# Kernel optimization log

Measured on AMD Instinct MI355X. Metric: run time of the kernel, lower is better.

Reference implementation:

```python
import jax, jax.numpy as jnp
import numpy as np
from jax import lax

N, CIN, COUT = 10000, 64, 32
RADIUS = 0.07
K = 32            # cap on neighbors per query (radius search truncated to K nearest)
KSIZE = 3         # kernel_size = [3,3,3]
NCELLS = KSIZE ** 3

# 8 trilinear corner offsets
_OFFS = np.array([[i, j, k] for i in (0, 1) for j in (0, 1) for k in (0, 1)], dtype=np.int32)  # (8,3)
_STRIDE = np.array([KSIZE * KSIZE, KSIZE, 1], dtype=np.int32)


def setup_inputs() -> dict:
    key = jax.random.key(0)
    k1, k2, k3 = jax.random.split(key, 3)
    points = jax.random.uniform(k1, (N, 3), dtype=jnp.float32)
    feats = jax.random.normal(k2, (N, CIN), dtype=jnp.float32)
    # ContinuousConv kernel: [3,3,3,Cin,Cout] flattened to [27,Cin,Cout]
    W = jax.random.normal(k3, (NCELLS, CIN, COUT), dtype=jnp.float32) * 0.05
    b = jnp.zeros((COUT,), dtype=jnp.float32)
    return {"feats": feats, "points": points, "W": W, "b": b}


def _neighbors(points):
    # squared pairwise distances (N,N); radius search truncated to K nearest
    sq = jnp.sum(points * points, axis=-1)
    d2 = sq[:, None] + sq[None, :] - 2.0 * (points @ points.T)
    neg_d2, idx = lax.top_k(-d2, K)           # (N,K)
    valid = (-neg_d2) <= RADIUS * RADIUS      # (N,K) bool
    return idx, valid


def _cconv(feats, points, W, b, idx, valid):
    nb_pos = points[idx]                      # (N,K,3) gather
    rel = (nb_pos - points[:, None, :]) / RADIUS   # normalized by half-extent -> unit ball
    # ball_to_cube_radial: v -> v * ||v||_2 / ||v||_inf  (0 at origin)
    l2 = jnp.linalg.norm(rel, axis=-1, keepdims=True)
    linf = jnp.max(jnp.abs(rel), axis=-1, keepdims=True)
    t = jnp.where(linf > 0, rel * (l2 / jnp.maximum(linf, 1e-12)), 0.0)  # in [-1,1]^3
    # map to kernel grid coords in [0, KSIZE-1]
    coords = (t + 1.0) * 0.5 * (KSIZE - 1)    # (N,K,3)
    c0 = jnp.clip(jnp.floor(coords), 0, KSIZE - 2)
    f = coords - c0                            # trilinear fractions, (N,K,3)
    offs = jnp.asarray(_OFFS)                  # (8,3)
    # trilinear weights (N,K,8)
    fw = jnp.where(offs[None, None] == 1, f[:, :, None, :], 1.0 - f[:, :, None, :])
    w8 = jnp.prod(fw, axis=-1)
    # flattened corner cell indices (N,K,8)
    cidx = jnp.sum((c0[:, :, None, :].astype(jnp.int32) + offs) * jnp.asarray(_STRIDE), axis=-1)
    onehot = jax.nn.one_hot(cidx, NCELLS, dtype=feats.dtype)        # (N,K,8,27)
    wmass = jnp.einsum('nke,nkej->nkj', w8, onehot)                 # (N,K,27)
    wmass = wmass * valid[:, :, None].astype(feats.dtype)
    nb_feats = feats[idx]                                           # (N,K,Cin)
    A = jnp.einsum('nkj,nkf->njf', wmass, nb_feats)                 # (N,27,Cin)
    out = jnp.einsum('njf,jfo->no', A, W)                           # (N,Cout)
    # normalize=True: divide by neighbor importance sum (count, window=None)
    nn = jnp.sum(valid.astype(feats.dtype), axis=-1)
    out = out / jnp.maximum(nn, 1.0)[:, None] + b
    return out


@jax.jit
def reference(feats, points, W, b):
    idx, valid = _neighbors(points)
    return _cconv(feats, points, W, b, idx, valid)
```

## Files before the change

kernel.cpp:

```cpp
#include <hip/hip_runtime.h>
#include <math.h>

#define N_PTS   10000
#define CIN     64
#define COUT    32
#define KCAP    32
#define RADIUSF 0.07f
#define NCELLS  27
#define QB      4
#define MAXC    48
#define GRES    14
#define GCELLS  (GRES * GRES * GRES)
#define CPAD    72
#define NSCAT   40
#define WT_ELEMS (NCELLS * COUT * CIN)

typedef __attribute__((ext_vector_type(8))) short         bf16x8_t;
typedef __attribute__((ext_vector_type(4))) float         f32x4_t;

__device__ __forceinline__ void cell_coords(float x, float y, float z,
                                            int& cx, int& cy, int& cz) {
    cx = (int)(x * (float)GRES); if (cx > GRES - 1) cx = GRES - 1; if (cx < 0) cx = 0;
    cy = (int)(y * (float)GRES); if (cy > GRES - 1) cy = GRES - 1; if (cy < 0) cy = 0;
    cz = (int)(z * (float)GRES); if (cz > GRES - 1) cz = GRES - 1; if (cz < 0) cz = 0;
}

__device__ __forceinline__ unsigned int f2bf_u(float x) {
    unsigned int u = __float_as_uint(x);
    return (u + 0x7FFFu + ((u >> 16) & 1u)) >> 16;
}

__global__ __launch_bounds__(1024) void k1_hist_scan(
    const float* __restrict__ pts,
    int* __restrict__ offsets,
    int* __restrict__ cursor)
{
    __shared__ int s_hist[GCELLS];
    __shared__ int s_wsum[16];
    const int t = threadIdx.x;
    const int lane = t & 63;
    const int wv   = t >> 6;

    for (int i = t; i < GCELLS; i += 1024) s_hist[i] = 0;
    __syncthreads();
    for (int i = t; i < N_PTS; i += 1024) {
        int cx, cy, cz;
        cell_coords(pts[3 * i], pts[3 * i + 1], pts[3 * i + 2], cx, cy, cz);
        atomicAdd(&s_hist[(cx * GRES + cy) * GRES + cz], 1);
    }
    __syncthreads();

    const int c0 = t * 3;
    int v0 = (c0 + 0 < GCELLS) ? s_hist[c0 + 0] : 0;
    int v1 = (c0 + 1 < GCELLS) ? s_hist[c0 + 1] : 0;
    int v2 = (c0 + 2 < GCELLS) ? s_hist[c0 + 2] : 0;
    const int local = v0 + v1 + v2;
    int inc = local;
    #pragma unroll
    for (int d = 1; d < 64; d <<= 1) {
        int up = __shfl_up(inc, d);
        if (lane >= d) inc += up;
    }
    if (lane == 63) s_wsum[wv] = inc;
    __syncthreads();
    if (t == 0) {
        int run = 0;
        #pragma unroll
        for (int i = 0; i < 16; ++i) { int tmp = s_wsum[i]; s_wsum[i] = run; run += tmp; }
    }
    __syncthreads();
    int base = s_wsum[wv] + (inc - local);
    if (c0 + 0 < GCELLS) { offsets[c0 + 0] = base; cursor[c0 + 0] = base; base += v0; }
    if (c0 + 1 < GCELLS) { offsets[c0 + 1] = base; cursor[c0 + 1] = base; base += v1; }
    if (c0 + 2 < GCELLS) { offsets[c0 + 2] = base; cursor[c0 + 2] = base; base += v2; }
    if (t == 0) offsets[GCELLS] = N_PTS;
}

__global__ __launch_bounds__(256) void k2_scatter_wt(
    const float* __restrict__ pts,
    const float* __restrict__ W,
    int*   __restrict__ cursor,
    int*   __restrict__ sorted,
    float* __restrict__ pts_s,
    unsigned short* __restrict__ Wt)
{
    const int b = blockIdx.x;
    const int t = threadIdx.x;

    if (b < NSCAT) {
        const int per = N_PTS / NSCAT;
        const int lo = b * per;
        const int hi = lo + per;
        for (int i = lo + t; i < hi; i += 256) {
            float x = pts[3 * i + 0], y = pts[3 * i + 1], z = pts[3 * i + 2];
            int cx, cy, cz;
            cell_coords(x, y, z, cx, cy, cz);
            int cell = (cx * GRES + cy) * GRES + cz;
            int pos = atomicAdd(&cursor[cell], 1);
            sorted[pos] = i;
            pts_s[3 * pos + 0] = x;
            pts_s[3 * pos + 1] = y;
            pts_s[3 * pos + 2] = z;
        }
    } else {
        __shared__ float tile[CIN * 33];
        const int cell = b - NSCAT;
        for (int idx = t; idx < CIN * COUT; idx += 256) {
            int f = idx >> 5, o = idx & 31;
            tile[f * 33 + o] = W[cell * (CIN * COUT) + idx];
        }
        __syncthreads();
        for (int idx = t; idx < CIN * COUT; idx += 256) {
            int o = idx >> 6, f = idx & 63;
            Wt[cell * (CIN * COUT) + idx] = (unsigned short)f2bf_u(tile[f * 33 + o]);
        }
    }
}

__global__ __launch_bounds__(256) void cconv_grid_mfma_kernel(
    const float* __restrict__ feats,
    const unsigned short* __restrict__ Wt,
    const float* __restrict__ bias,
    const int*   __restrict__ offsets,
    const int*   __restrict__ sorted,
    const float* __restrict__ pts_s,
    float* __restrict__ out)
{
    const int tid  = threadIdx.x;
    const int lane = tid & 63;
    const int wave = tid >> 6;

    __shared__ __align__(16) unsigned short sAb[QB][NCELLS + 1][CPAD];
    __shared__ __align__(16) float s_pool[QB][4][MAXC];
    __shared__ int   s_idx[QB][MAXC];
    __shared__ int   s_org[QB][MAXC];
    __shared__ int   s_sel[QB][KCAP];
    __shared__ int   s_cnt[QB];
    __shared__ int   s_qi[QB];
    __shared__ int   s_nn[QB];

    if (lane == 0) s_cnt[wave] = 0;

    const int q_flat = blockIdx.x * QB + wave;
    const int qi = sorted[q_flat];
    const float qx = pts_s[3 * q_flat + 0];
    const float qy = pts_s[3 * q_flat + 1];
    const float qz = pts_s[3 * q_flat + 2];
    const float sqn = qx * qx + qy * qy + qz * qz;
    const float r2 = RADIUSF * RADIUSF;

    int cx, cy, cz;
    cell_coords(qx, qy, qz, cx, cy, cz);

    int zlo = cz - 1; if (zlo < 0) zlo = 0;
    int zhi = cz + 1; if (zhi > GRES - 1) zhi = GRES - 1;
    int ss[9], sl[9];
    #pragma unroll
    for (int dxi = 0; dxi < 3; ++dxi) {
        #pragma unroll
        for (int dyi = 0; dyi < 3; ++dyi) {
            const int ii = dxi * 3 + dyi;
            int cxx = cx + dxi - 1, cyy = cy + dyi - 1;
            bool ok = (cxx >= 0) && (cxx <= GRES - 1) && (cyy >= 0) && (cyy <= GRES - 1);
            int row = ((ok ? cxx : 0) * GRES + (ok ? cyy : 0)) * GRES;
            int s = offsets[row + zlo];
            int e = offsets[row + zhi + 1];
            ss[ii] = s;
            sl[ii] = ok ? (e - s) : 0;
        }
    }
    int cum[10];
    cum[0] = 0;
    #pragma unroll
    for (int ii = 0; ii < 9; ++ii) cum[ii + 1] = cum[ii] + sl[ii];
    const int T = cum[9];

    for (int t = lane; t < T; t += 64) {
        int gidx = 0;
        #pragma unroll
        for (int ii = 0; ii < 9; ++ii) {
            bool in = (t >= cum[ii]) && (t < cum[ii + 1]);
            int cand = ss[ii] + (t - cum[ii]);
            gidx = in ? cand : gidx;
        }
        float x = pts_s[3 * gidx + 0];
        float y = pts_s[3 * gidx + 1];
        float z = pts_s[3 * gidx + 2];
        float sqj = x * x + y * y + z * z;
        float dot = qx * x + qy * y + qz * z;
        float d2 = (sqn + sqj) - 2.0f * dot;
        if (d2 <= r2) {
            int pos = atomicAdd(&s_cnt[wave], 1);
            if (pos < MAXC) {
                s_pool[wave][0][pos] = d2;
                s_pool[wave][1][pos] = x;
                s_pool[wave][2][pos] = y;
                s_pool[wave][3][pos] = z;
                s_idx[wave][pos] = gidx;
            }
        }
    }

    int M = s_cnt[wave]; if (M > MAXC) M = MAXC;
    const int cnt = (M > KCAP) ? KCAP : M;
    const bool over = (M > KCAP);

    if (lane < M) s_org[wave][lane] = sorted[s_idx[wave][lane]];

    if (over) {
        if (lane < M) {
            float dc = s_pool[wave][0][lane];
            int   ic = s_org[wave][lane];
            int rank = 0;
            for (int m = 0; m < M; ++m) {
                float dm = s_pool[wave][0][m];
                int   im = s_org[wave][m];
                rank += (dm < dc || (dm == dc && im < ic)) ? 1 : 0;
            }
            if (rank < KCAP) s_sel[wave][rank] = lane;
        }
    }
    if (lane == 0) { s_qi[wave] = qi; s_nn[wave] = cnt; }

    float* w9w = (float*)&sAb[wave][0][0];
    if (lane < cnt) {
        int slot = over ? s_sel[wave][lane] : lane;
        float x = s_pool[wave][1][slot];
        float y = s_pool[wave][2][slot];
        float z = s_pool[wave][3][slot];
        int   j = s_org[wave][slot];
        float rx = (x - qx) / RADIUSF;
        float ry = (y - qy) / RADIUSF;
        float rz = (z - qz) / RADIUSF;
        float l2 = sqrtf(rx * rx + ry * ry + rz * rz);
        float ax = fabsf(rx), ay = fabsf(ry), az = fabsf(rz);
        float linf = fmaxf(fmaxf(ax, ay), az);
        float s = (linf > 0.0f) ? (l2 / fmaxf(linf, 1e-12f)) : 0.0f;
        float tx = rx * s, ty = ry * s, tz = rz * s;
        float cxf = (tx + 1.0f) * 0.5f * 2.0f;
        float cyf = (ty + 1.0f) * 0.5f * 2.0f;
        float czf = (tz + 1.0f) * 0.5f * 2.0f;
        float c0x = fminf(fmaxf(floorf(cxf), 0.0f), 1.0f);
        float c0y = fminf(fmaxf(floorf(cyf), 0.0f), 1.0f);
        float c0z = fminf(fmaxf(floorf(czf), 0.0f), 1.0f);
        float fx = cxf - c0x;
        float fy = cyf - c0y;
        float fz = czf - c0z;
        int i0 = (int)c0x, i1 = (int)c0y, i2 = (int)c0z;
        float gx0 = 1.0f - fx, gx1 = fx;
        float gy0 = 1.0f - fy, gy1 = fy;
        float gz0 = 1.0f - fz, gz1 = fz;
        float* wp = w9w + lane * 12;
        wp[0] = i0 ? 0.0f : gx0;  wp[1] = i0 ? gx0 : gx1;  wp[2] = i0 ? gx1 : 0.0f;
        wp[3] = i1 ? 0.0f : gy0;  wp[4] = i1 ? gy0 : gy1;  wp[5] = i1 ? gy1 : 0.0f;
        wp[6] = i2 ? 0.0f : gz0;  wp[7] = i2 ? gz0 : gz1;  wp[8] = i2 ? gz1 : 0.0f;
        wp[9] = __int_as_float(j * CIN);
    }

    float a[NCELLS];
    #pragma unroll
    for (int c = 0; c < NCELLS; ++c) a[c] = 0.0f;

    if (cnt > 0) {
        float fvA = feats[__float_as_int(w9w[9]) + lane];
        float fvB = 0.0f;
        if (cnt > 1) fvB = feats[__float_as_int(w9w[12 + 9]) + lane];
        for (int k = 0; k < cnt; ++k) {
            const float* wp = w9w + k * 12;
            float wxv[3] = {wp[0], wp[1], wp[2]};
            float wyv[3] = {wp[3], wp[4], wp[5]};
            float wz0 = wp[6], wz1 = wp[7], wz2 = wp[8];
            float fv_cur = fvA;
            fvA = fvB;
            if (k + 2 < cnt) fvB = feats[__float_as_int(w9w[(k + 2) * 12 + 9]) + lane];
            float pzv[3] = {wz0 * fv_cur, wz1 * fv_cur, wz2 * fv_cur};
            #pragma unroll
            for (int ci = 0; ci < 3; ++ci) {
                #pragma unroll
                for (int cj = 0; cj < 3; ++cj) {
                    float wxy = wxv[ci] * wyv[cj];
                    #pragma unroll
                    for (int ck = 0; ck < 3; ++ck) {
                        a[ci * 9 + cj * 3 + ck] = fmaf(wxy, pzv[ck], a[ci * 9 + cj * 3 + ck]);
                    }
                }
            }
        }
    }
    #pragma unroll
    for (int c = 0; c < NCELLS; ++c) sAb[wave][c][lane] = (unsigned short)f2bf_u(a[c]);
    sAb[wave][NCELLS][lane] = 0;
    __syncthreads();

    float (*sC)[QB][COUT] = (float (*)[QB][COUT])&s_pool[0][0][0];
    f32x4_t acc0 = {0.f, 0.f, 0.f, 0.f};
    f32x4_t acc1 = {0.f, 0.f, 0.f, 0.f};
    const int r  = lane & 15;
    const int kg = lane >> 4;
    #pragma unroll
    for (int it = 0; it < 14; ++it) {
        const int s5 = wave + it * 4;
        const int c  = s5 >> 1;
        const int f0 = (s5 & 1) << 5;
        const int cw = (c < NCELLS) ? c : 0;
        bf16x8_t af = {};
        if (r < QB) af = *(const bf16x8_t*)&sAb[r][c][f0 + kg * 8];
        const unsigned short* wp0 = Wt + ((cw * COUT + r     ) * CIN + f0 + kg * 8);
        const unsigned short* wp1 = Wt + ((cw * COUT + 16 + r) * CIN + f0 + kg * 8);
        bf16x8_t bf0 = *(const bf16x8_t*)wp0;
        bf16x8_t bf1 = *(const bf16x8_t*)wp1;
        acc0 = __builtin_amdgcn_mfma_f32_16x16x32_bf16(af, bf0, acc0, 0, 0, 0);
        acc1 = __builtin_amdgcn_mfma_f32_16x16x32_bf16(af, bf1, acc1, 0, 0, 0);
    }
    if (lane < 16) {
        #pragma unroll
        for (int j = 0; j < QB; ++j) {
            sC[wave][j][lane]      = acc0[j];
            sC[wave][j][16 + lane] = acc1[j];
        }
    }
    __syncthreads();

    if (tid < QB * COUT) {
        int q = tid >> 5, o = tid & 31;
        float v = sC[0][q][o] + sC[1][q][o] + sC[2][q][o] + sC[3][q][o];
        float nn = (float)s_nn[q];
        out[s_qi[q] * COUT + o] = v / fmaxf(nn, 1.0f) + bias[o];
    }
}

__global__ __launch_bounds__(64) void cconv_fused_kernel(
    const float* __restrict__ feats,
    const float* __restrict__ points,
    const float* __restrict__ W,
    const float* __restrict__ bias,
    float* __restrict__ out)
{
    const int n    = blockIdx.x;
    const int lane = threadIdx.x;

    __shared__ float sA[NCELLS][CIN];
    __shared__ float s_d2[128];
    __shared__ int   s_idx[128];
    __shared__ int   s_rank[128];
    __shared__ int   s_sel[KCAP];
    __shared__ int   s_cnt;

    if (lane == 0) s_cnt = 0;
    for (int c = lane; c < NCELLS * CIN; c += 64) ((float*)sA)[c] = 0.0f;
    __syncthreads();

    const float qx = points[3 * n + 0];
    const float qy = points[3 * n + 1];
    const float qz = points[3 * n + 2];
    const float sqn = qx * qx + qy * qy + qz * qz;
    const float r2 = RADIUSF * RADIUSF;

    for (int j = lane; j < N_PTS; j += 64) {
        float x = points[3 * j + 0];
        float y = points[3 * j + 1];
        float z = points[3 * j + 2];
        float sqj = x * x + y * y + z * z;
        float dot = qx * x + qy * y + qz * z;
        float d2 = (sqn + sqj) - 2.0f * dot;
        if (d2 <= r2) {
            int pos = atomicAdd(&s_cnt, 1);
            if (pos < 128) { s_d2[pos] = d2; s_idx[pos] = j; }
        }
    }
    __syncthreads();

    int M = s_cnt; if (M > 128) M = 128;
    int cnt;
    if (M > KCAP) {
        for (int c = lane; c < M; c += 64) {
            float dc = s_d2[c]; int ic = s_idx[c]; int rank = 0;
            for (int m = 0; m < M; ++m) {
                float dm = s_d2[m]; int im = s_idx[m];
                rank += (dm < dc || (dm == dc && im < ic)) ? 1 : 0;
            }
            s_rank[c] = rank;
        }
        __syncthreads();
        for (int c = lane; c < M; c += 64) {
            int r = s_rank[c];
            if (r < KCAP) s_sel[r] = s_idx[c];
        }
        __syncthreads();
        cnt = KCAP;
    } else cnt = M;
    const int* nbr = (M > KCAP) ? s_sel : s_idx;

    for (int k = 0; k < cnt; ++k) {
        int j = nbr[k];
        float x = points[3 * j + 0];
        float y = points[3 * j + 1];
        float z = points[3 * j + 2];
        float rx = (x - qx) / RADIUSF;
        float ry = (y - qy) / RADIUSF;
        float rz = (z - qz) / RADIUSF;
        float l2 = sqrtf(rx * rx + ry * ry + rz * rz);
        float ax = fabsf(rx), ay = fabsf(ry), az = fabsf(rz);
        float linf = fmaxf(fmaxf(ax, ay), az);
        float s = (linf > 0.0f) ? (l2 / fmaxf(linf, 1e-12f)) : 0.0f;
        float tx = rx * s, ty = ry * s, tz = rz * s;
        float cxf = (tx + 1.0f) * 0.5f * 2.0f;
        float cyf = (ty + 1.0f) * 0.5f * 2.0f;
        float czf = (tz + 1.0f) * 0.5f * 2.0f;
        float c0x = fminf(fmaxf(floorf(cxf), 0.0f), 1.0f);
        float c0y = fminf(fmaxf(floorf(cyf), 0.0f), 1.0f);
        float c0z = fminf(fmaxf(floorf(czf), 0.0f), 1.0f);
        float fx = cxf - c0x, fy = cyf - c0y, fz = czf - c0z;
        int i0 = (int)c0x, i1 = (int)c0y, i2 = (int)c0z;
        int base = i0 * 9 + i1 * 3 + i2;
        float gx0 = 1.0f - fx, gx1 = fx;
        float gy0 = 1.0f - fy, gy1 = fy;
        float gz0 = 1.0f - fz, gz1 = fz;
        float featv = feats[j * CIN + lane];
        sA[base + 0 ][lane] += (gx0 * gy0) * gz0 * featv;
        sA[base + 1 ][lane] += (gx0 * gy0) * gz1 * featv;
        sA[base + 3 ][lane] += (gx0 * gy1) * gz0 * featv;
        sA[base + 4 ][lane] += (gx0 * gy1) * gz1 * featv;
        sA[base + 9 ][lane] += (gx1 * gy0) * gz0 * featv;
        sA[base + 10][lane] += (gx1 * gy0) * gz1 * featv;
        sA[base + 12][lane] += (gx1 * gy1) * gz0 * featv;
        sA[base + 13][lane] += (gx1 * gy1) * gz1 * featv;
    }
    __syncthreads();

    const int o    = lane & 31;
    const int half = lane >> 5;
    const int c_begin = half ? 14 : 0;
    const int c_end   = half ? 27 : 14;
    float acc = 0.0f;
    for (int cell = c_begin; cell < c_end; ++cell) {
        const float* __restrict__ Wrow = W + (cell * CIN) * COUT + o;
        #pragma unroll 8
        for (int f = 0; f < CIN; ++f) acc += sA[cell][f] * Wrow[f * COUT];
    }
    acc += __shfl_xor(acc, 32);
    if (lane < COUT) {
        float nn = (float)cnt;
        out[n * COUT + lane] = acc / fmaxf(nn, 1.0f) + bias[lane];
    }
}

extern "C" void kernel_launch(void* const* d_in, const int* in_sizes, int n_in,
                              void* d_out, int out_size, void* d_ws, size_t ws_size,
                              hipStream_t stream) {
    const float* feats  = (const float*)d_in[0];
    const float* points = (const float*)d_in[1];
    const float* W      = (const float*)d_in[2];
    const float* bias   = (const float*)d_in[3];
    float* out = (float*)d_out;

    const size_t wt_bytes = (size_t)WT_ELEMS * sizeof(unsigned short);
    const size_t need     = wt_bytes
                          + (size_t)(GCELLS + 1 + GCELLS + N_PTS) * sizeof(int)
                          + (size_t)3 * N_PTS * sizeof(float);

    if (ws_size >= need) {
        unsigned short* Wt = (unsigned short*)d_ws;
        int* offsets = (int*)((char*)d_ws + wt_bytes);
        int* cursor  = offsets + GCELLS + 1;
        int* sorted  = cursor + GCELLS;
        float* pts_s = (float*)(sorted + N_PTS);

        k1_hist_scan<<<1, 1024, 0, stream>>>(points, offsets, cursor);
        k2_scatter_wt<<<NSCAT + NCELLS, 256, 0, stream>>>(points, W, cursor, sorted, pts_s, Wt);
        cconv_grid_mfma_kernel<<<N_PTS / QB, QB * 64, 0, stream>>>(
            feats, Wt, bias, offsets, sorted, pts_s, out);
    } else {
        cconv_fused_kernel<<<N_PTS, 64, 0, stream>>>(feats, points, W, bias, out);
    }
}
```

Before: 115.3 us.

## Process eight queries per block, prefetch MFMA operands, move weight transpose earlier

Doubles queries per block from four to eight (512 threads), so the bf16 MFMA tile uses 8 of its 16 rows and each wave covers half as many K-steps. The MFMA loop now loads the A and B fragments of the next step before issuing the current MFMAs, to hide load latency. The weight transpose to bf16 moves from the scatter kernel into the histogram kernel as extra blocks, so it runs alongside the single-block scan. Larger blocks mean more shared memory per block and fewer blocks, which can lower occupancy and leave fewer blocks to balance the work.

```diff
diff --git a/kernel.cpp b/kernel.cpp
--- a/kernel.cpp
+++ b/kernel.cpp
@@ -7,7 +7,7 @@
 #define KCAP    32
 #define RADIUSF 0.07f
 #define NCELLS  27
-#define QB      4
+#define QB      8
 #define MAXC    48
 #define GRES    14
 #define GCELLS  (GRES * GRES * GRES)
@@ -30,14 +30,33 @@
     return (u + 0x7FFFu + ((u >> 16) & 1u)) >> 16;
 }
 
-__global__ __launch_bounds__(1024) void k1_hist_scan(
+__global__ __launch_bounds__(1024) void k1_hist_scan_wt(
     const float* __restrict__ pts,
+    const float* __restrict__ W,
     int* __restrict__ offsets,
-    int* __restrict__ cursor)
+    int* __restrict__ cursor,
+    unsigned short* __restrict__ Wt)
 {
+    const int t = threadIdx.x;
+    const int b = blockIdx.x;
+
+    if (b >= 1) {
+        __shared__ float tile[CIN * 33];
+        const int cell = b - 1;
+        for (int idx = t; idx < CIN * COUT; idx += 1024) {
+            int f = idx >> 5, o = idx & 31;
+            tile[f * 33 + o] = W[cell * (CIN * COUT) + idx];
+        }
+        __syncthreads();
+        for (int idx = t; idx < CIN * COUT; idx += 1024) {
+            int o = idx >> 6, f = idx & 63;
+            Wt[cell * (CIN * COUT) + idx] = (unsigned short)f2bf_u(tile[f * 33 + o]);
+        }
+        return;
+    }
+
     __shared__ int s_hist[GCELLS];
     __shared__ int s_wsum[16];
-    const int t = threadIdx.x;
     const int lane = t & 63;
     const int wv   = t >> 6;
 
@@ -76,48 +95,31 @@
     if (t == 0) offsets[GCELLS] = N_PTS;
 }
 
-__global__ __launch_bounds__(256) void k2_scatter_wt(
+__global__ __launch_bounds__(256) void k2_scatter(
     const float* __restrict__ pts,
-    const float* __restrict__ W,
     int*   __restrict__ cursor,
     int*   __restrict__ sorted,
-    float* __restrict__ pts_s,
-    unsigned short* __restrict__ Wt)
+    float* __restrict__ pts_s)
 {
     const int b = blockIdx.x;
     const int t = threadIdx.x;
-
-    if (b < NSCAT) {
-        const int per = N_PTS / NSCAT;
-        const int lo = b * per;
-        const int hi = lo + per;
-        for (int i = lo + t; i < hi; i += 256) {
-            float x = pts[3 * i + 0], y = pts[3 * i + 1], z = pts[3 * i + 2];
-            int cx, cy, cz;
-            cell_coords(x, y, z, cx, cy, cz);
-            int cell = (cx * GRES + cy) * GRES + cz;
-            int pos = atomicAdd(&cursor[cell], 1);
-            sorted[pos] = i;
-            pts_s[3 * pos + 0] = x;
-            pts_s[3 * pos + 1] = y;
-            pts_s[3 * pos + 2] = z;
-        }
-    } else {
-        __shared__ float tile[CIN * 33];
-        const int cell = b - NSCAT;
-        for (int idx = t; idx < CIN * COUT; idx += 256) {
-            int f = idx >> 5, o = idx & 31;
-            tile[f * 33 + o] = W[cell * (CIN * COUT) + idx];
-        }
-        __syncthreads();
-        for (int idx = t; idx < CIN * COUT; idx += 256) {
-            int o = idx >> 6, f = idx & 63;
-            Wt[cell * (CIN * COUT) + idx] = (unsigned short)f2bf_u(tile[f * 33 + o]);
-        }
-    }
-}
-
-__global__ __launch_bounds__(256) void cconv_grid_mfma_kernel(
+    const int per = N_PTS / NSCAT;
+    const int lo = b * per;
+    const int hi = lo + per;
+    for (int i = lo + t; i < hi; i += 256) {
+        float x = pts[3 * i + 0], y = pts[3 * i + 1], z = pts[3 * i + 2];
+        int cx, cy, cz;
+        cell_coords(x, y, z, cx, cy, cz);
+        int cell = (cx * GRES + cy) * GRES + cz;
+        int pos = atomicAdd(&cursor[cell], 1);
+        sorted[pos] = i;
+        pts_s[3 * pos + 0] = x;
+        pts_s[3 * pos + 1] = y;
+        pts_s[3 * pos + 2] = z;
+    }
+}
+
+__global__ __launch_bounds__(512) void cconv_grid_mfma_kernel(
     const float* __restrict__ feats,
     const unsigned short* __restrict__ Wt,
     const float* __restrict__ bias,
@@ -131,13 +133,15 @@
     const int wave = tid >> 6;
 
     __shared__ __align__(16) unsigned short sAb[QB][NCELLS + 1][CPAD];
-    __shared__ __align__(16) float s_pool[QB][4][MAXC];
+    __shared__ __align__(16) float s_scratch[2048];
     __shared__ int   s_idx[QB][MAXC];
     __shared__ int   s_org[QB][MAXC];
     __shared__ int   s_sel[QB][KCAP];
     __shared__ int   s_cnt[QB];
     __shared__ int   s_qi[QB];
     __shared__ int   s_nn[QB];
+
+    float (*s_pool)[4][MAXC] = (float (*)[4][MAXC])s_scratch;
 
     if (lane == 0) s_cnt[wave] = 0;
 
@@ -292,38 +296,58 @@
     sAb[wave][NCELLS][lane] = 0;
     __syncthreads();
 
-    float (*sC)[QB][COUT] = (float (*)[QB][COUT])&s_pool[0][0][0];
     f32x4_t acc0 = {0.f, 0.f, 0.f, 0.f};
     f32x4_t acc1 = {0.f, 0.f, 0.f, 0.f};
     const int r  = lane & 15;
     const int kg = lane >> 4;
+
+    #define STEP_ADDR(it, cvar, fvar, cwvar)                                   \
+        const int s5_##it = wave + (it) * 8;                                   \
+        const int cvar = s5_##it >> 1;                                         \
+        const int fvar = (s5_##it & 1) << 5;                                   \
+        const int cwvar = (cvar < NCELLS) ? cvar : 0;
+
+    STEP_ADDR(0, c_0, f_0, cw_0)
+    bf16x8_t aCur = {}, bCur0, bCur1;
+    if (r < QB) aCur = *(const bf16x8_t*)&sAb[r][c_0][f_0 + kg * 8];
+    bCur0 = *(const bf16x8_t*)(Wt + ((cw_0 * COUT + r     ) * CIN + f_0 + kg * 8));
+    bCur1 = *(const bf16x8_t*)(Wt + ((cw_0 * COUT + 16 + r) * CIN + f_0 + kg * 8));
+
     #pragma unroll
-    for (int it = 0; it < 14; ++it) {
-        const int s5 = wave + it * 4;
-        const int c  = s5 >> 1;
-        const int f0 = (s5 & 1) << 5;
-        const int cw = (c < NCELLS) ? c : 0;
-        bf16x8_t af = {};
-        if (r < QB) af = *(const bf16x8_t*)&sAb[r][c][f0 + kg * 8];
-        const unsigned short* wp0 = Wt + ((cw * COUT + r     ) * CIN + f0 + kg * 8);
-        const unsigned short* wp1 = Wt + ((cw * COUT + 16 + r) * CIN + f0 + kg * 8);
-        bf16x8_t bf0 = *(const bf16x8_t*)wp0;
-        bf16x8_t bf1 = *(const bf16x8_t*)wp1;
-        acc0 = __builtin_amdgcn_mfma_f32_16x16x32_bf16(af, bf0, acc0, 0, 0, 0);
-        acc1 = __builtin_amdgcn_mfma_f32_16x16x32_bf16(af, bf1, acc1, 0, 0, 0);
-    }
-    if (lane < 16) {
+    for (int it = 0; it < 7; ++it) {
+        bf16x8_t aNxt = {}, bNxt0 = {}, bNxt1 = {};
+        if (it + 1 < 7) {
+            const int s5n = wave + (it + 1) * 8;
+            const int cn  = s5n >> 1;
+            const int fn  = (s5n & 1) << 5;
+            const int cwn = (cn < NCELLS) ? cn : 0;
+            if (r < QB) aNxt = *(const bf16x8_t*)&sAb[r][cn][fn + kg * 8];
+            bNxt0 = *(const bf16x8_t*)(Wt + ((cwn * COUT + r     ) * CIN + fn + kg * 8));
+            bNxt1 = *(const bf16x8_t*)(Wt + ((cwn * COUT + 16 + r) * CIN + fn + kg * 8));
+        }
+        acc0 = __builtin_amdgcn_mfma_f32_16x16x32_bf16(aCur, bCur0, acc0, 0, 0, 0);
+        acc1 = __builtin_amdgcn_mfma_f32_16x16x32_bf16(aCur, bCur1, acc1, 0, 0, 0);
+        aCur = aNxt; bCur0 = bNxt0; bCur1 = bNxt1;
+    }
+    #undef STEP_ADDR
+
+    float (*sC)[QB][COUT] = (float (*)[QB][COUT])s_scratch;
+    if (lane < 32) {
+        int qrow = (lane >> 4) * 4;
+        int o = lane & 15;
         #pragma unroll
-        for (int j = 0; j < QB; ++j) {
-            sC[wave][j][lane]      = acc0[j];
-            sC[wave][j][16 + lane] = acc1[j];
+        for (int j = 0; j < 4; ++j) {
+            sC[wave][qrow + j][o]      = acc0[j];
+            sC[wave][qrow + j][16 + o] = acc1[j];
         }
     }
     __syncthreads();
 
     if (tid < QB * COUT) {
         int q = tid >> 5, o = tid & 31;
-        float v = sC[0][q][o] + sC[1][q][o] + sC[2][q][o] + sC[3][q][o];
+        float v = 0.0f;
+        #pragma unroll
+        for (int w = 0; w < QB; ++w) v += sC[w][q][o];
         float nn = (float)s_nn[q];
         out[s_qi[q] * COUT + o] = v / fmaxf(nn, 1.0f) + bias[o];
     }
@@ -466,8 +490,8 @@
         int* sorted  = cursor + GCELLS;
         float* pts_s = (float*)(sorted + N_PTS);
 
-        k1_hist_scan<<<1, 1024, 0, stream>>>(points, offsets, cursor);
-        k2_scatter_wt<<<NSCAT + NCELLS, 256, 0, stream>>>(points, W, cursor, sorted, pts_s, Wt);
+        k1_hist_scan_wt<<<1 + NCELLS, 1024, 0, stream>>>(points, W, offsets, cursor, Wt);
+        k2_scatter<<<NSCAT, 256, 0, stream>>>(points, cursor, sorted, pts_s);
         cconv_grid_mfma_kernel<<<N_PTS / QB, QB * 64, 0, stream>>>(
             feats, Wt, bias, offsets, sorted, pts_s, out);
     } else {
```

Result: faster. 105.7 us (-8.4%).
